# Kernel tuning notes

Measured on AMD Instinct MI355X. Metric: run time of the kernel, lower is better.

The kernel has to match this reference:

```python
import jax, jax.numpy as jnp
import numpy as np

N, F, O, E = 2048, 128, 128, 16


def setup_inputs() -> dict:
    key = jax.random.key(0)
    ks = jax.random.split(key, 6)
    x = jax.random.normal(ks[0], (N, F), dtype=jnp.float32)
    # two supports (normalized adjacency-like dense matrices)
    support = jax.random.uniform(ks[1], (2, N, N), dtype=jnp.float32)
    edge_feature = jax.random.normal(ks[2], (N, N, E), dtype=jnp.float32)
    # glorot-ish scale for edge weight and dense weights
    weight_edge = jax.random.normal(ks[3], (N, N, E), dtype=jnp.float32) * 0.05
    bias_edge = jnp.zeros((N, N), dtype=jnp.float32)
    glorot = float(np.sqrt(6.0 / (F + O)))
    w0 = jax.random.uniform(ks[4], (F, O), dtype=jnp.float32, minval=-glorot, maxval=glorot)
    w1 = jax.random.uniform(ks[5], (F, O), dtype=jnp.float32, minval=-glorot, maxval=glorot)
    b = jnp.zeros((O,), dtype=jnp.float32)
    return {"x": x, "support": support, "edge_feature": edge_feature,
            "weight_edge": weight_edge, "bias_edge": bias_edge,
            "w0": w0, "w1": w1, "b": b}


def reference(x, support, edge_feature, weight_edge, bias_edge, w0, w1, b):
    # support branch 0: plain GCN propagation  (SpMM expressed dense)
    pre0 = x @ w0                      # [N, O]
    s0 = support[0] @ pre0             # [N, O]
    # support branch 1: edge-feature gated propagation
    pre1 = x @ w1                      # [N, O]
    # per-pair dot of edge features with per-pair weights -> [N, N] gate
    edge = jax.nn.sigmoid(jnp.einsum('nme,nme->nm', edge_feature, weight_edge) + bias_edge)
    s1 = (edge * support[1]) @ pre1    # gated adjacency matmul, [N, O]
    out = s0 + s1 + b                  # add_n + bias
    return jax.nn.relu(out)
```

## Files before the change

kernel.cpp:

```cpp
#include <hip/hip_runtime.h>
#include <math.h>

#define N 2048
#define F 128
#define O 128
#define E 16

#define BN 32
#define BK 32
#define KC 8
#define MK (N / KC)
#define STEPS (MK / BK)
#define APAD 40
#define BPAD 40

typedef __attribute__((ext_vector_type(8))) short          shortx8;
typedef __attribute__((ext_vector_type(8))) unsigned short u16x8;
typedef __attribute__((ext_vector_type(4))) float          floatx4;

static __device__ __forceinline__ unsigned short f2bf(float f) {
    unsigned int u = __float_as_uint(f);
    unsigned int r = (u + 0x7FFFu + ((u >> 16) & 1u)) >> 16;
    return (unsigned short)r;
}

__global__ __launch_bounds__(128)
void pre_gemm(const float* __restrict__ x,
              const float* __restrict__ w0,
              const float* __restrict__ w1,
              unsigned short* __restrict__ pre_bf) {
    const int n = blockIdx.x;
    const int b = blockIdx.y;
    const int o = threadIdx.x;
    const float* __restrict__ w = b ? w1 : w0;
    __shared__ float xs[F];
    xs[o] = x[(size_t)n * F + o];
    __syncthreads();
    float acc = 0.f;
#pragma unroll 8
    for (int k = 0; k < F; ++k)
        acc += xs[k] * w[(size_t)k * O + o];
    pre_bf[(size_t)b * N * O + (size_t)n * O + o] = f2bf(acc);
}

__global__ __launch_bounds__(256)
void transpose_pre(const unsigned short* __restrict__ pre_bf,
                   unsigned short* __restrict__ preT) {
    __shared__ unsigned short tile[64][65];
    const int n0 = blockIdx.x * 64, o0 = blockIdx.y * 64;
    const size_t base = (size_t)blockIdx.z * N * O;
    const int t = threadIdx.x;
    const int r = t >> 2, q = t & 3;
    const unsigned short* src = pre_bf + base + (size_t)(n0 + r) * O + o0 + q * 16;
    u16x8 v0 = *(const u16x8*)(src);
    u16x8 v1 = *(const u16x8*)(src + 8);
#pragma unroll
    for (int j = 0; j < 8; ++j) {
        tile[q * 16 + j][r]     = v0[j];
        tile[q * 16 + 8 + j][r] = v1[j];
    }
    __syncthreads();
    u16x8 w0v, w1v;
#pragma unroll
    for (int j = 0; j < 8; ++j) {
        w0v[j] = tile[r][q * 16 + j];
        w1v[j] = tile[r][q * 16 + 8 + j];
    }
    unsigned short* dst = preT + base + (size_t)(o0 + r) * N + n0 + q * 16;
    *(u16x8*)(dst)     = w0v;
    *(u16x8*)(dst + 8) = w1v;
}


struct Pref {
    float4 e0[4], e1[4], w0[4], w1[4];
    float  be0, be1, s00, s01, s10, s11;
    u16x8  bv0, bv1;
};

__device__ __forceinline__ void load_step(
    const float* __restrict__ ef, const float* __restrict__ we,
    const float* __restrict__ be, const float* __restrict__ S0,
    const float* __restrict__ sup1, const unsigned short* __restrict__ preT,
    size_t pix0, size_t sbase, int m0, Pref& P)
{
    const size_t pixA = pix0 + (size_t)m0;
    const size_t pixB = pixA + (size_t)16 * N;
    const float4* eA = (const float4*)(ef + pixA * E);
    const float4* wA = (const float4*)(we + pixA * E);
    const float4* eB = (const float4*)(ef + pixB * E);
    const float4* wB = (const float4*)(we + pixB * E);
#pragma unroll
    for (int j = 0; j < 4; ++j) {
        P.e0[j] = eA[j]; P.w0[j] = wA[j];
        P.e1[j] = eB[j]; P.w1[j] = wB[j];
    }
    P.be0 = be[pixA]; P.s00 = S0[pixA]; P.s10 = sup1[pixA];
    P.be1 = be[pixB]; P.s01 = S0[pixB]; P.s11 = sup1[pixB];
    const size_t src = sbase + (size_t)m0;
    P.bv0 = *(const u16x8*)(preT + src);
    P.bv1 = *(const u16x8*)(preT + (size_t)O * N + src);
}

__device__ __forceinline__ void produce(
    const Pref& P, int nn0, int mm0, int bo, int bq,
    unsigned short* aS, unsigned short* aG,
    unsigned short* B0, unsigned short* B1)
{
    float v0 = 0.f, v1 = 0.f;
#pragma unroll
    for (int j = 0; j < 4; ++j) {
        v0 += P.e0[j].x * P.w0[j].x + P.e0[j].y * P.w0[j].y
            + P.e0[j].z * P.w0[j].z + P.e0[j].w * P.w0[j].w;
        v1 += P.e1[j].x * P.w1[j].x + P.e1[j].y * P.w1[j].y
            + P.e1[j].z * P.w1[j].z + P.e1[j].w * P.w1[j].w;
    }
    const float g0 = (1.f / (1.f + __expf(-(v0 + P.be0)))) * P.s10;
    const float g1 = (1.f / (1.f + __expf(-(v1 + P.be1)))) * P.s11;
    aG[nn0 * APAD + mm0]        = f2bf(g0);
    aG[(nn0 + 16) * APAD + mm0] = f2bf(g1);
    aS[nn0 * APAD + mm0]        = f2bf(P.s00);
    aS[(nn0 + 16) * APAD + mm0] = f2bf(P.s01);
    *(u16x8*)(B0 + bo * BPAD + bq * 8) = P.bv0;
    *(u16x8*)(B1 + bo * BPAD + bq * 8) = P.bv1;
}

__device__ __forceinline__ void mfma_step(
    const unsigned short* aS, const unsigned short* aG,
    const unsigned short* B0, const unsigned short* B1,
    int arow, int kg, int col0, floatx4& acc0, floatx4& acc1)
{
    const shortx8 a_s = *(const shortx8*)(aS + arow * APAD + kg * 8);
    const shortx8 a_g = *(const shortx8*)(aG + arow * APAD + kg * 8);
    const shortx8 b00 = *(const shortx8*)(B0 + col0 * BPAD + kg * 8);
    const shortx8 b10 = *(const shortx8*)(B1 + col0 * BPAD + kg * 8);
    const shortx8 b01 = *(const shortx8*)(B0 + (col0 + 16) * BPAD + kg * 8);
    const shortx8 b11 = *(const shortx8*)(B1 + (col0 + 16) * BPAD + kg * 8);
    acc0 = __builtin_amdgcn_mfma_f32_16x16x32_bf16(a_s, b00, acc0, 0, 0, 0);
    acc0 = __builtin_amdgcn_mfma_f32_16x16x32_bf16(a_g, b10, acc0, 0, 0, 0);
    acc1 = __builtin_amdgcn_mfma_f32_16x16x32_bf16(a_s, b01, acc1, 0, 0, 0);
    acc1 = __builtin_amdgcn_mfma_f32_16x16x32_bf16(a_g, b11, acc1, 0, 0, 0);
}

__global__ __launch_bounds__(512, 4)
void fused_gemm(const float* __restrict__ sup,
                const float* __restrict__ ef,
                const float* __restrict__ we,
                const float* __restrict__ be,
                const unsigned short* __restrict__ preT,
                float* __restrict__ partial) {
    __shared__ unsigned short aS0[BN * APAD], aG0[BN * APAD];
    __shared__ unsigned short B00[O * BPAD],  B10[O * BPAD];
    __shared__ unsigned short aS1[BN * APAD], aG1[BN * APAD];
    __shared__ unsigned short B01[O * BPAD],  B11[O * BPAD];

    const int tid = threadIdx.x;
    const int bx  = blockIdx.x;
    const int rb  = bx & 63;
    const int kc  = bx >> 6;
    const int n0     = rb * BN;
    const int m_base = kc * MK;

    const float* __restrict__ S0   = sup;
    const float* __restrict__ sup1 = sup + (size_t)N * N;

    const int lane = tid & 63;
    const int wid  = tid >> 6;
    const int wrow = wid >> 2;
    const int wcol = wid & 3;

    const int nn0 = tid >> 5;
    const int mm0 = tid & 31;
    const int bo  = tid >> 2;
    const int bq  = tid & 3;

    const size_t pix0  = (size_t)(n0 + nn0) * N + (size_t)(m_base + mm0);
    const size_t sbase = (size_t)bo * N + (size_t)(m_base + bq * 8);

    const int arow = wrow * 16 + (lane & 15);
    const int kg   = lane >> 4;
    const int col0 = wcol * 32 + (lane & 15);

    floatx4 acc0 = {0.f, 0.f, 0.f, 0.f};
    floatx4 acc1 = {0.f, 0.f, 0.f, 0.f};

    Pref P;
    load_step(ef, we, be, S0, sup1, preT, pix0, sbase, 0, P);
    produce(P, nn0, mm0, bo, bq, aS0, aG0, B00, B10);
    load_step(ef, we, be, S0, sup1, preT, pix0, sbase, BK, P);
    __syncthreads();

#pragma unroll 1
    for (int s = 0; s < STEPS; s += 2) {
        produce(P, nn0, mm0, bo, bq, aS1, aG1, B01, B11);
        if (s + 2 < STEPS)
            load_step(ef, we, be, S0, sup1, preT, pix0, sbase, (s + 2) * BK, P);
        mfma_step(aS0, aG0, B00, B10, arow, kg, col0, acc0, acc1);
        __syncthreads();
        if (s + 2 < STEPS) {
            produce(P, nn0, mm0, bo, bq, aS0, aG0, B00, B10);
            if (s + 3 < STEPS)
                load_step(ef, we, be, S0, sup1, preT, pix0, sbase, (s + 3) * BK, P);
        }
        mfma_step(aS1, aG1, B01, B11, arow, kg, col0, acc0, acc1);
        __syncthreads();
    }

    const int prow = (lane >> 4) * 4;
    const int pcol = wcol * 32 + (lane & 15);
    float* dst = partial + (size_t)kc * (N * O)
               + (size_t)(n0 + wrow * 16 + prow) * O + pcol;
#pragma unroll
    for (int j = 0; j < 4; ++j) {
        dst[(size_t)j * O]      = acc0[j];
        dst[(size_t)j * O + 16] = acc1[j];
    }
}

__global__ __launch_bounds__(256)
void reduce_out(const float* __restrict__ partial,
                const float* __restrict__ bias,
                float* __restrict__ out) {
    const int i4 = blockIdx.x * 256 + threadIdx.x;
    const float4* p = (const float4*)partial;
    float4 r = p[i4];
#pragma unroll
    for (int j = 1; j < KC; ++j) {
        const float4 a = p[i4 + (size_t)j * 65536];
        r.x += a.x; r.y += a.y; r.z += a.z; r.w += a.w;
    }
    const float4 bb = ((const float4*)bias)[i4 & 31];
    float4 o;
    o.x = fmaxf(r.x + bb.x, 0.f);
    o.y = fmaxf(r.y + bb.y, 0.f);
    o.z = fmaxf(r.z + bb.z, 0.f);
    o.w = fmaxf(r.w + bb.w, 0.f);
    ((float4*)out)[i4] = o;
}

extern "C" void kernel_launch(void* const* d_in, const int* in_sizes, int n_in,
                              void* d_out, int out_size, void* d_ws, size_t ws_size,
                              hipStream_t stream) {
    const float* x   = (const float*)d_in[0];
    const float* sup = (const float*)d_in[1];
    const float* ef  = (const float*)d_in[2];
    const float* we  = (const float*)d_in[3];
    const float* be  = (const float*)d_in[4];
    const float* w0  = (const float*)d_in[5];
    const float* w1  = (const float*)d_in[6];
    const float* b   = (const float*)d_in[7];
    float* out = (float*)d_out;

    unsigned short* pre_bf = (unsigned short*)d_ws;
    unsigned short* preT   = pre_bf + 2 * (size_t)N * O;
    float* partial = (float*)(preT + 2 * (size_t)N * O);

    pre_gemm<<<dim3(N, 2), 128, 0, stream>>>(x, w0, w1, pre_bf);
    transpose_pre<<<dim3(N / 64, O / 64, 2), 256, 0, stream>>>(pre_bf, preT);
    fused_gemm<<<KC * 64, 512, 0, stream>>>(sup, ef, we, be, preT, partial);
    reduce_out<<<256, 256, 0, stream>>>(partial, b, out);
}
```

Measured before the change: 148.6 us.

## Coalesce edge-feature loads across 4-lane groups and drop register prefetch

Edge-feature and weight loads are restructured so that four consecutive lanes each read one float4 of the same pixel, with a shuffle reduction combining the partial dot products. The goal is fully coalesced, contiguous global reads instead of each thread striding through 64-byte per-pixel records. The register-held prefetch of the next step is removed, so loads are issued inside produce just before their use. This lowers register pressure but gives up explicit load/compute overlap, and adds shuffles plus redundant per-lane sigmoid work.

```diff
diff --git a/kernel.cpp b/kernel.cpp
--- a/kernel.cpp
+++ b/kernel.cpp
@@ -72,59 +72,6 @@
 }
 
 
-struct Pref {
-    float4 e0[4], e1[4], w0[4], w1[4];
-    float  be0, be1, s00, s01, s10, s11;
-    u16x8  bv0, bv1;
-};
-
-__device__ __forceinline__ void load_step(
-    const float* __restrict__ ef, const float* __restrict__ we,
-    const float* __restrict__ be, const float* __restrict__ S0,
-    const float* __restrict__ sup1, const unsigned short* __restrict__ preT,
-    size_t pix0, size_t sbase, int m0, Pref& P)
-{
-    const size_t pixA = pix0 + (size_t)m0;
-    const size_t pixB = pixA + (size_t)16 * N;
-    const float4* eA = (const float4*)(ef + pixA * E);
-    const float4* wA = (const float4*)(we + pixA * E);
-    const float4* eB = (const float4*)(ef + pixB * E);
-    const float4* wB = (const float4*)(we + pixB * E);
-#pragma unroll
-    for (int j = 0; j < 4; ++j) {
-        P.e0[j] = eA[j]; P.w0[j] = wA[j];
-        P.e1[j] = eB[j]; P.w1[j] = wB[j];
-    }
-    P.be0 = be[pixA]; P.s00 = S0[pixA]; P.s10 = sup1[pixA];
-    P.be1 = be[pixB]; P.s01 = S0[pixB]; P.s11 = sup1[pixB];
-    const size_t src = sbase + (size_t)m0;
-    P.bv0 = *(const u16x8*)(preT + src);
-    P.bv1 = *(const u16x8*)(preT + (size_t)O * N + src);
-}
-
-__device__ __forceinline__ void produce(
-    const Pref& P, int nn0, int mm0, int bo, int bq,
-    unsigned short* aS, unsigned short* aG,
-    unsigned short* B0, unsigned short* B1)
-{
-    float v0 = 0.f, v1 = 0.f;
-#pragma unroll
-    for (int j = 0; j < 4; ++j) {
-        v0 += P.e0[j].x * P.w0[j].x + P.e0[j].y * P.w0[j].y
-            + P.e0[j].z * P.w0[j].z + P.e0[j].w * P.w0[j].w;
-        v1 += P.e1[j].x * P.w1[j].x + P.e1[j].y * P.w1[j].y
-            + P.e1[j].z * P.w1[j].z + P.e1[j].w * P.w1[j].w;
-    }
-    const float g0 = (1.f / (1.f + __expf(-(v0 + P.be0)))) * P.s10;
-    const float g1 = (1.f / (1.f + __expf(-(v1 + P.be1)))) * P.s11;
-    aG[nn0 * APAD + mm0]        = f2bf(g0);
-    aG[(nn0 + 16) * APAD + mm0] = f2bf(g1);
-    aS[nn0 * APAD + mm0]        = f2bf(P.s00);
-    aS[(nn0 + 16) * APAD + mm0] = f2bf(P.s01);
-    *(u16x8*)(B0 + bo * BPAD + bq * 8) = P.bv0;
-    *(u16x8*)(B1 + bo * BPAD + bq * 8) = P.bv1;
-}
-
 __device__ __forceinline__ void mfma_step(
     const unsigned short* aS, const unsigned short* aG,
     const unsigned short* B0, const unsigned short* B1,
@@ -154,28 +101,25 @@
     __shared__ unsigned short aS1[BN * APAD], aG1[BN * APAD];
     __shared__ unsigned short B01[O * BPAD],  B11[O * BPAD];
 
-    const int tid = threadIdx.x;
-    const int bx  = blockIdx.x;
-    const int rb  = bx & 63;
-    const int kc  = bx >> 6;
+    const int t  = threadIdx.x;
+    const int bx = blockIdx.x;
+    const int rb = bx & 63;
+    const int kc = bx >> 6;
     const int n0     = rb * BN;
     const int m_base = kc * MK;
 
     const float* __restrict__ S0   = sup;
     const float* __restrict__ sup1 = sup + (size_t)N * N;
-
-    const int lane = tid & 63;
-    const int wid  = tid >> 6;
+    const float4* __restrict__ efv = (const float4*)ef;
+    const float4* __restrict__ wev = (const float4*)we;
+
+    const int lane = t & 63;
+    const int wid  = t >> 6;
     const int wrow = wid >> 2;
     const int wcol = wid & 3;
 
-    const int nn0 = tid >> 5;
-    const int mm0 = tid & 31;
-    const int bo  = tid >> 2;
-    const int bq  = tid & 3;
-
-    const size_t pix0  = (size_t)(n0 + nn0) * N + (size_t)(m_base + mm0);
-    const size_t sbase = (size_t)bo * N + (size_t)(m_base + bq * 8);
+    const int sub = t & 3;
+    const int grp = t >> 2;
 
     const int arow = wrow * 16 + (lane & 15);
     const int kg   = lane >> 4;
@@ -184,24 +128,46 @@
     floatx4 acc0 = {0.f, 0.f, 0.f, 0.f};
     floatx4 acc1 = {0.f, 0.f, 0.f, 0.f};
 
-    Pref P;
-    load_step(ef, we, be, S0, sup1, preT, pix0, sbase, 0, P);
-    produce(P, nn0, mm0, bo, bq, aS0, aG0, B00, B10);
-    load_step(ef, we, be, S0, sup1, preT, pix0, sbase, BK, P);
+    auto produce = [&](int m0, unsigned short* aS, unsigned short* aG,
+                       unsigned short* B0, unsigned short* B1) {
+        {
+            const size_t src = (size_t)grp * N + (size_t)(m0 + sub * 8);
+            *(u16x8*)(B0 + grp * BPAD + sub * 8) = *(const u16x8*)(preT + src);
+            *(u16x8*)(B1 + grp * BPAD + sub * 8) =
+                *(const u16x8*)(preT + (size_t)O * N + src);
+        }
+        const size_t pbase = (size_t)n0 * N + (size_t)m0;
+#pragma unroll
+        for (int r = 0; r < 8; ++r) {
+            const int p  = r * 128 + grp;
+            const int nn = p >> 5, mm = p & 31;
+            const size_t pix = pbase + (size_t)nn * N + mm;
+            const float4 e = efv[pix * 4 + sub];
+            const float4 w = wev[pix * 4 + sub];
+            float v = e.x * w.x + e.y * w.y + e.z * w.z + e.w * w.w;
+            v += __shfl_xor(v, 1);
+            v += __shfl_xor(v, 2);
+            const float g = (1.f / (1.f + __expf(-(v + be[pix])))) * sup1[pix];
+            if (sub == 0) aG[nn * APAD + mm] = f2bf(g);
+        }
+#pragma unroll
+        for (int r = 0; r < 2; ++r) {
+            const int p  = r * 512 + t;
+            const int nn = p >> 5, mm = p & 31;
+            aS[nn * APAD + mm] = f2bf(S0[pbase + (size_t)nn * N + mm]);
+        }
+    };
+
+    produce(m_base, aS0, aG0, B00, B10);
     __syncthreads();
 
 #pragma unroll 1
     for (int s = 0; s < STEPS; s += 2) {
-        produce(P, nn0, mm0, bo, bq, aS1, aG1, B01, B11);
-        if (s + 2 < STEPS)
-            load_step(ef, we, be, S0, sup1, preT, pix0, sbase, (s + 2) * BK, P);
+        produce(m_base + (s + 1) * BK, aS1, aG1, B01, B11);
         mfma_step(aS0, aG0, B00, B10, arow, kg, col0, acc0, acc1);
         __syncthreads();
-        if (s + 2 < STEPS) {
-            produce(P, nn0, mm0, bo, bq, aS0, aG0, B00, B10);
-            if (s + 3 < STEPS)
-                load_step(ef, we, be, S0, sup1, preT, pix0, sbase, (s + 3) * BK, P);
-        }
+        if (s + 2 < STEPS)
+            produce(m_base + (s + 2) * BK, aS0, aG0, B00, B10);
         mfma_step(aS1, aG1, B01, B11, arow, kg, col0, acc0, acc1);
         __syncthreads();
     }
```

New measurement: 189.2 us. 27.3% more time.
